# Kernel tuning notes

Measured on AMD Instinct MI355X. Metric: run time of the kernel, lower is better.

The kernel has to match this reference:

```python
import jax, jax.numpy as jnp
import numpy as np

INPUT_DIM = 64
INNER_DIM = 64
BATCH = 32768


def setup_inputs() -> dict:
    key = jax.random.key(0)
    ks = jax.random.split(key, 9)
    D, I = INPUT_DIM, INNER_DIM
    s1 = 1.0  # Linear(1, inner): fan_in=1
    s2 = 1.0 / np.sqrt(I)
    sg1 = 1.0 / np.sqrt(D * I)
    sg2 = 1.0 / np.sqrt(I)
    return {
        "x": jax.random.normal(ks[0], (BATCH, D), dtype=jnp.float32),
        # per-feature psi params, stacked over feature dim D
        "W1": jax.random.uniform(ks[1], (D, I), jnp.float32, -s1, s1),   # Linear(1, inner) weight
        "b1": jax.random.uniform(ks[2], (D, I), jnp.float32, -s1, s1),
        "W2": jax.random.uniform(ks[3], (D, I, I), jnp.float32, -s2, s2),  # Linear(inner, inner)
        "b2": jax.random.uniform(ks[4], (D, I), jnp.float32, -s2, s2),
        # g params
        "Wg1": jax.random.uniform(ks[5], (D * I, I), jnp.float32, -sg1, sg1),
        "bg1": jax.random.uniform(ks[6], (I,), jnp.float32, -sg1, sg1),
        "Wg2": jax.random.uniform(ks[7], (I, 1), jnp.float32, -sg2, sg2),
        "bg2": jax.random.uniform(ks[8], (1,), jnp.float32, -sg2, sg2),
    }


def reference(x, W1, b1, W2, b2, Wg1, bg1, Wg2, bg2):
    B = x.shape[0]
    # all psi_i first layers as one broadcasted outer product: [B, D, I]
    h = jnp.tanh(x[:, :, None] * W1[None, :, :] + b1[None, :, :])
    # per-feature second Linear(inner, inner): batched matmul over D
    psi = jnp.einsum("bdi,dio->bdo", h, W2) + b2[None, :, :]
    psi_concat = psi.reshape(B, -1)  # [B, D*I] == torch.cat over features
    hg = jnp.tanh(psi_concat @ Wg1 + bg1)
    out = hg @ Wg2 + bg2  # [B, 1]
    return out
```

## Files before the change

kernel.cpp:

```cpp
#include <hip/hip_runtime.h>
#include <stdint.h>

#define BATCH 32768
#define TANH_C 2.8853900817779268f

typedef __attribute__((ext_vector_type(8))) short short8;
typedef __attribute__((ext_vector_type(4))) float f32x4;
typedef __attribute__((ext_vector_type(4))) unsigned int u32x4;

__device__ __forceinline__ uint16_t bf16_rtne(float f) {
    union { float f; uint32_t u; } v; v.f = f;
    uint32_t u = v.u;
    u += 0x7fffu + ((u >> 16) & 1u);
    return (uint16_t)(u >> 16);
}

#if defined(__has_builtin)
#if __has_builtin(__builtin_amdgcn_cvt_pk_bf16_f32)
#define HAVE_CVT_PK_BF16 1
#endif
#endif

__device__ __forceinline__ uint32_t pack2_bf16(float a, float b) {
#ifdef HAVE_CVT_PK_BF16
    auto v = __builtin_amdgcn_cvt_pk_bf16_f32(a, b);
    uint32_t r; __builtin_memcpy(&r, &v, 4); return r;
#else
    return (uint32_t)bf16_rtne(a) | ((uint32_t)bf16_rtne(b) << 16);
#endif
}

__device__ __forceinline__ uint32_t tanh2_pack(float a, float b) {
    float ea = __builtin_amdgcn_exp2f(a);
    float eb = __builtin_amdgcn_exp2f(b);
    float da = 1.0f + ea, db = 1.0f + eb;
    float ir = __builtin_amdgcn_rcpf(da * db);
    float ha = fmaf(-2.0f * db, ir, 1.0f);
    float hb = fmaf(-2.0f * da, ir, 1.0f);
    return pack2_bf16(ha, hb);
}

__device__ __forceinline__ float fast_tanh(float x) {
    float e = __builtin_amdgcn_exp2f(x * TANH_C);
    return 1.0f - 2.0f * __builtin_amdgcn_rcpf(1.0f + e);
}

__global__ __launch_bounds__(512) void kol_pack(const float* __restrict__ W2,
                                                const float* __restrict__ Wg1,
                                                const float* __restrict__ b2,
                                                uint16_t* __restrict__ Bp,
                                                float* __restrict__ cgpart) {
    __shared__ __align__(16) float w2t[64 * 65];
    __shared__ __align__(16) float g1s[64 * 64];

    const int t = threadIdx.x;
    const int d = blockIdx.x;

    for (int f = t * 4; f < 4096; f += 2048) {
        float4 v = *(const float4*)&W2[(size_t)d * 4096 + f];
        int j = f >> 6, o = f & 63;
        w2t[(o + 0) * 65 + j] = v.x;
        w2t[(o + 1) * 65 + j] = v.y;
        w2t[(o + 2) * 65 + j] = v.z;
        w2t[(o + 3) * 65 + j] = v.w;
        *(float4*)&g1s[f] = *(const float4*)&Wg1[(size_t)d * 4096 + f];
    }
    __syncthreads();

    const int jg = t >> 6;
    const int n  = t & 63;
    float acc[8];
#pragma unroll
    for (int i = 0; i < 8; ++i) acc[i] = 0.f;

#pragma unroll 4
    for (int o = 0; o < 64; ++o) {
        float g = g1s[o * 64 + n];
        const float* w = &w2t[o * 65 + jg * 8];
#pragma unroll
        for (int jj = 0; jj < 8; ++jj) acc[jj] = fmaf(w[jj], g, acc[jj]);
    }

    u32x4 pk;
    pk.x = pack2_bf16(acc[0], acc[1]);
    pk.y = pack2_bf16(acc[2], acc[3]);
    pk.z = pack2_bf16(acc[4], acc[5]);
    pk.w = pack2_bf16(acc[6], acc[7]);
    int off = ((d * 2 + (jg >> 2)) * 4 + (n >> 4)) * 64 + (jg & 3) * 16 + (n & 15);
    ((u32x4*)Bp)[off] = pk;

    if (t < 64) {
        float a = 0.f;
        const float* b2d = &b2[(size_t)d * 64];
#pragma unroll 4
        for (int o = 0; o < 64; ++o)
            a = fmaf(b2d[o], g1s[o * 64 + t], a);
        cgpart[d * 64 + t] = a;
    }
}

__global__ __launch_bounds__(256) void kol_reduce_cg(const float* __restrict__ cgpart,
                                                     const float* __restrict__ bg1,
                                                     float* __restrict__ cg) {
    __shared__ float red[4][64];
    const int t = threadIdx.x;
    const int n = t & 63, seg = t >> 6;
    float a = 0.f;
#pragma unroll 4
    for (int d = seg * 16; d < seg * 16 + 16; ++d)
        a += cgpart[d * 64 + n];
    red[seg][n] = a;
    __syncthreads();
    if (t < 64)
        cg[n] = bg1[n] + red[0][n] + red[1][n] + red[2][n] + red[3][n];
}

__global__ __launch_bounds__(512, 4) void kol_main(
    const float* __restrict__ x, const float* __restrict__ W1, const float* __restrict__ b1,
    const uint16_t* __restrict__ Bp, const float* __restrict__ cg,
    const float* __restrict__ Wg2, const float* __restrict__ bg2f,
    float* __restrict__ out) {
    __shared__ __align__(16) float xs[64 * 68];
    __shared__ __align__(16) float w1s[4096];
    __shared__ __align__(16) float b1s[4096];

    const int tid = threadIdx.x;
    const int wave = tid >> 6, lane = tid & 63;
    const int quad = lane >> 4, lm = lane & 15;
    const int w4 = wave & 3, kh = wave >> 2;
    const int rowbase = blockIdx.x * 64;

#pragma unroll
    for (int ff = 0; ff < 2; ++ff) {
        int f = tid * 4 + ff * 2048;
        int r = f >> 6, c = f & 63;
        float4 v = *(const float4*)&x[(size_t)(rowbase + r) * 64 + c];
        v.x *= TANH_C; v.y *= TANH_C; v.z *= TANH_C; v.w *= TANH_C;
        *(float4*)&xs[r * 68 + c] = v;
        *(float4*)&w1s[f] = *(const float4*)&W1[f];
        float4 b = *(const float4*)&b1[f];
        b.x *= TANH_C; b.y *= TANH_C; b.z *= TANH_C; b.w *= TANH_C;
        *(float4*)&b1s[f] = b;
    }
    __syncthreads();

    f32x4 acc[4];
#pragma unroll
    for (int nt = 0; nt < 4; ++nt) acc[nt] = (f32x4){0.f, 0.f, 0.f, 0.f};

    const int dlo = kh * 32;
    const int myrow = w4 * 16 + lm;
    const float* xrow = &xs[myrow * 68];
    const short8* bbase = (const short8*)Bp + lane;

    short8 bf[8];
    {
        const short8* bp0 = bbase + (size_t)dlo * 512;
#pragma unroll
        for (int i = 0; i < 8; ++i) bf[i] = bp0[i * 64];
    }

#pragma unroll 2
    for (int dd = 0; dd < 32; ++dd) {
        const int d = dlo + dd;
        short8 bn[8];
        const short8* bpn = bbase + (size_t)(dlo + ((dd + 1) & 31)) * 512;
#pragma unroll
        for (int i = 0; i < 8; ++i) bn[i] = bpn[i * 64];

        const float xv = xrow[d];
        const float* wq = &w1s[d * 64 + quad * 8];
        const float* bq = &b1s[d * 64 + quad * 8];
        float4 wA = *(const float4*)&wq[0];
        float4 wB = *(const float4*)&wq[4];
        float4 wC = *(const float4*)&wq[32];
        float4 wD = *(const float4*)&wq[36];
        float4 bA = *(const float4*)&bq[0];
        float4 bB = *(const float4*)&bq[4];
        float4 bC = *(const float4*)&bq[32];
        float4 bD = *(const float4*)&bq[36];

        union { short8 s; uint32_t u[4]; } a0, a1;
        a0.u[0] = tanh2_pack(fmaf(xv, wA.x, bA.x), fmaf(xv, wA.y, bA.y));
        a0.u[1] = tanh2_pack(fmaf(xv, wA.z, bA.z), fmaf(xv, wA.w, bA.w));
        a0.u[2] = tanh2_pack(fmaf(xv, wB.x, bB.x), fmaf(xv, wB.y, bB.y));
        a0.u[3] = tanh2_pack(fmaf(xv, wB.z, bB.z), fmaf(xv, wB.w, bB.w));
        a1.u[0] = tanh2_pack(fmaf(xv, wC.x, bC.x), fmaf(xv, wC.y, bC.y));
        a1.u[1] = tanh2_pack(fmaf(xv, wC.z, bC.z), fmaf(xv, wC.w, bC.w));
        a1.u[2] = tanh2_pack(fmaf(xv, wD.x, bD.x), fmaf(xv, wD.y, bD.y));
        a1.u[3] = tanh2_pack(fmaf(xv, wD.z, bD.z), fmaf(xv, wD.w, bD.w));

#pragma unroll
        for (int nt = 0; nt < 4; ++nt)
            acc[nt] = __builtin_amdgcn_mfma_f32_16x16x32_bf16(a0.s, bf[nt], acc[nt], 0, 0, 0);
#pragma unroll
        for (int nt = 0; nt < 4; ++nt)
            acc[nt] = __builtin_amdgcn_mfma_f32_16x16x32_bf16(a1.s, bf[4 + nt], acc[nt], 0, 0, 0);

#pragma unroll
        for (int i = 0; i < 8; ++i) bf[i] = bn[i];
    }

    __syncthreads();
    float* cmb = xs;
    if (kh == 1) {
        int cb = (w4 * 64 + lane) * 17;
#pragma unroll
        for (int nt = 0; nt < 4; ++nt) *(f32x4*)&cmb[cb + nt * 4] = acc[nt];
    }
    __syncthreads();

    if (kh == 0) {
        int cb = (w4 * 64 + lane) * 17;
#pragma unroll
        for (int nt = 0; nt < 4; ++nt) {
            f32x4 o = *(const f32x4*)&cmb[cb + nt * 4];
            acc[nt] = acc[nt] + o;
        }
        float wg2v[4], cgv[4];
#pragma unroll
        for (int nt = 0; nt < 4; ++nt) {
            wg2v[nt] = Wg2[nt * 16 + lm];
            cgv[nt]  = cg[nt * 16 + lm];
        }
        const float bg2 = bg2f[0];
#pragma unroll
        for (int r = 0; r < 4; ++r) {
            float s = 0.f;
#pragma unroll
            for (int nt = 0; nt < 4; ++nt)
                s += wg2v[nt] * fast_tanh(acc[nt][r] + cgv[nt]);
            s += __shfl_xor(s, 1, 64);
            s += __shfl_xor(s, 2, 64);
            s += __shfl_xor(s, 4, 64);
            s += __shfl_xor(s, 8, 64);
            if (lm == 0) {
                int row = rowbase + w4 * 16 + quad * 4 + r;
                out[row] = s + bg2;
            }
        }
    }
}

extern "C" void kernel_launch(void* const* d_in, const int* in_sizes, int n_in,
                              void* d_out, int out_size, void* d_ws, size_t ws_size,
                              hipStream_t stream) {
    const float* x   = (const float*)d_in[0];
    const float* W1  = (const float*)d_in[1];
    const float* b1  = (const float*)d_in[2];
    const float* W2  = (const float*)d_in[3];
    const float* b2  = (const float*)d_in[4];
    const float* Wg1 = (const float*)d_in[5];
    const float* bg1 = (const float*)d_in[6];
    const float* Wg2 = (const float*)d_in[7];
    const float* bg2 = (const float*)d_in[8];
    float* out = (float*)d_out;

    uint16_t* Bp  = (uint16_t*)d_ws;
    float* cg     = (float*)((char*)d_ws + 4096 * 64 * 2);
    float* cgpart = out;

    kol_pack<<<64, 512, 0, stream>>>(W2, Wg1, b2, Bp, cgpart);
    kol_reduce_cg<<<1, 256, 0, stream>>>(cgpart, bg1, cg);
    kol_main<<<BATCH / 64, 512, 0, stream>>>(x, W1, b1, Bp, cg, Wg2, bg2, out);
}
```

Baseline: 126.9 us.

## Switch main kernel to 32x32x16 MFMA with 4-way K split across waves

```diff
diff --git a/kernel.cpp b/kernel.cpp
--- a/kernel.cpp
+++ b/kernel.cpp
@@ -6,6 +6,7 @@
 
 typedef __attribute__((ext_vector_type(8))) short short8;
 typedef __attribute__((ext_vector_type(4))) float f32x4;
+typedef __attribute__((ext_vector_type(16))) float f32x16;
 typedef __attribute__((ext_vector_type(4))) unsigned int u32x4;
 
 __device__ __forceinline__ uint16_t bf16_rtne(float f) {
@@ -86,7 +87,7 @@
     pk.y = pack2_bf16(acc[2], acc[3]);
     pk.z = pack2_bf16(acc[4], acc[5]);
     pk.w = pack2_bf16(acc[6], acc[7]);
-    int off = ((d * 2 + (jg >> 2)) * 4 + (n >> 4)) * 64 + (jg & 3) * 16 + (n & 15);
+    int off = ((d * 4 + (jg >> 1)) * 2 + (n >> 5)) * 64 + ((jg & 1) << 5) + (n & 31);
     ((u32x4*)Bp)[off] = pk;
 
     if (t < 64) {
@@ -120,14 +121,15 @@
     const uint16_t* __restrict__ Bp, const float* __restrict__ cg,
     const float* __restrict__ Wg2, const float* __restrict__ bg2f,
     float* __restrict__ out) {
-    __shared__ __align__(16) float xs[64 * 68];
-    __shared__ __align__(16) float w1s[4096];
-    __shared__ __align__(16) float b1s[4096];
+    __shared__ __align__(16) float smem[12544];
+    float* xs  = smem;
+    float* w1s = smem + 4352;
+    float* b1s = smem + 8448;
 
     const int tid = threadIdx.x;
     const int wave = tid >> 6, lane = tid & 63;
-    const int quad = lane >> 4, lm = lane & 15;
-    const int w4 = wave & 3, kh = wave >> 2;
+    const int nn = lane & 31, hi = lane >> 5;
+    const int rg = wave & 1, kq = wave >> 1;
     const int rowbase = blockIdx.x * 64;
 
 #pragma unroll
@@ -144,100 +146,98 @@
     }
     __syncthreads();
 
-    f32x4 acc[4];
-#pragma unroll
-    for (int nt = 0; nt < 4; ++nt) acc[nt] = (f32x4){0.f, 0.f, 0.f, 0.f};
-
-    const int dlo = kh * 32;
-    const int myrow = w4 * 16 + lm;
-    const float* xrow = &xs[myrow * 68];
-    const short8* bbase = (const short8*)Bp + lane;
-
-    short8 bf[8];
-    {
-        const short8* bp0 = bbase + (size_t)dlo * 512;
-#pragma unroll
-        for (int i = 0; i < 8; ++i) bf[i] = bp0[i * 64];
-    }
+    f32x16 acc0 = {0.f}, acc1 = {0.f};
+#pragma unroll
+    for (int i = 0; i < 16; ++i) { acc0[i] = 0.f; acc1[i] = 0.f; }
+
+    const u32x4* bp = (const u32x4*)Bp + lane;
+    const float* xcol = &xs[(rg * 32 + nn) * 68];
 
 #pragma unroll 2
-    for (int dd = 0; dd < 32; ++dd) {
-        const int d = dlo + dd;
-        short8 bn[8];
-        const short8* bpn = bbase + (size_t)(dlo + ((dd + 1) & 31)) * 512;
-#pragma unroll
-        for (int i = 0; i < 8; ++i) bn[i] = bpn[i * 64];
-
-        const float xv = xrow[d];
-        const float* wq = &w1s[d * 64 + quad * 8];
-        const float* bq = &b1s[d * 64 + quad * 8];
-        float4 wA = *(const float4*)&wq[0];
-        float4 wB = *(const float4*)&wq[4];
-        float4 wC = *(const float4*)&wq[32];
-        float4 wD = *(const float4*)&wq[36];
-        float4 bA = *(const float4*)&bq[0];
-        float4 bB = *(const float4*)&bq[4];
-        float4 bC = *(const float4*)&bq[32];
-        float4 bD = *(const float4*)&bq[36];
-
-        union { short8 s; uint32_t u[4]; } a0, a1;
-        a0.u[0] = tanh2_pack(fmaf(xv, wA.x, bA.x), fmaf(xv, wA.y, bA.y));
-        a0.u[1] = tanh2_pack(fmaf(xv, wA.z, bA.z), fmaf(xv, wA.w, bA.w));
-        a0.u[2] = tanh2_pack(fmaf(xv, wB.x, bB.x), fmaf(xv, wB.y, bB.y));
-        a0.u[3] = tanh2_pack(fmaf(xv, wB.z, bB.z), fmaf(xv, wB.w, bB.w));
-        a1.u[0] = tanh2_pack(fmaf(xv, wC.x, bC.x), fmaf(xv, wC.y, bC.y));
-        a1.u[1] = tanh2_pack(fmaf(xv, wC.z, bC.z), fmaf(xv, wC.w, bC.w));
-        a1.u[2] = tanh2_pack(fmaf(xv, wD.x, bD.x), fmaf(xv, wD.y, bD.y));
-        a1.u[3] = tanh2_pack(fmaf(xv, wD.z, bD.z), fmaf(xv, wD.w, bD.w));
-
-#pragma unroll
-        for (int nt = 0; nt < 4; ++nt)
-            acc[nt] = __builtin_amdgcn_mfma_f32_16x16x32_bf16(a0.s, bf[nt], acc[nt], 0, 0, 0);
-#pragma unroll
-        for (int nt = 0; nt < 4; ++nt)
-            acc[nt] = __builtin_amdgcn_mfma_f32_16x16x32_bf16(a1.s, bf[4 + nt], acc[nt], 0, 0, 0);
-
-#pragma unroll
-        for (int i = 0; i < 8; ++i) bf[i] = bn[i];
-    }
-
-    __syncthreads();
-    float* cmb = xs;
-    if (kh == 1) {
-        int cb = (w4 * 64 + lane) * 17;
-#pragma unroll
-        for (int nt = 0; nt < 4; ++nt) *(f32x4*)&cmb[cb + nt * 4] = acc[nt];
-    }
-    __syncthreads();
-
-    if (kh == 0) {
-        int cb = (w4 * 64 + lane) * 17;
-#pragma unroll
-        for (int nt = 0; nt < 4; ++nt) {
-            f32x4 o = *(const f32x4*)&cmb[cb + nt * 4];
-            acc[nt] = acc[nt] + o;
-        }
-        float wg2v[4], cgv[4];
-#pragma unroll
-        for (int nt = 0; nt < 4; ++nt) {
-            wg2v[nt] = Wg2[nt * 16 + lm];
-            cgv[nt]  = cg[nt * 16 + lm];
-        }
+    for (int dd = 0; dd < 16; ++dd) {
+        const int d = kq * 16 + dd;
+        const u32x4* bfp = bp + (size_t)d * 512;
+        u32x4 bfr[8];
+#pragma unroll
+        for (int i = 0; i < 8; ++i) bfr[i] = bfp[i * 64];
+
+        const float xv = xcol[d];
+        short8 afr[4];
+#pragma unroll
+        for (int c = 0; c < 4; ++c) {
+            const float* wq = &w1s[d * 64 + c * 16 + hi * 8];
+            const float* bq = &b1s[d * 64 + c * 16 + hi * 8];
+            float4 w0 = *(const float4*)&wq[0];
+            float4 w1v = *(const float4*)&wq[4];
+            float4 b0 = *(const float4*)&bq[0];
+            float4 b1v = *(const float4*)&bq[4];
+            union { short8 s; uint32_t u[4]; } a;
+            a.u[0] = tanh2_pack(fmaf(xv, w0.x, b0.x), fmaf(xv, w0.y, b0.y));
+            a.u[1] = tanh2_pack(fmaf(xv, w0.z, b0.z), fmaf(xv, w0.w, b0.w));
+            a.u[2] = tanh2_pack(fmaf(xv, w1v.x, b1v.x), fmaf(xv, w1v.y, b1v.y));
+            a.u[3] = tanh2_pack(fmaf(xv, w1v.z, b1v.z), fmaf(xv, w1v.w, b1v.w));
+            afr[c] = a.s;
+        }
+#pragma unroll
+        for (int c = 0; c < 4; ++c) {
+            union { u32x4 u; short8 s; } b0c, b1c;
+            b0c.u = bfr[c * 2 + 0];
+            b1c.u = bfr[c * 2 + 1];
+            acc0 = __builtin_amdgcn_mfma_f32_32x32x16_bf16(afr[c], b0c.s, acc0, 0, 0, 0);
+            acc1 = __builtin_amdgcn_mfma_f32_32x32x16_bf16(afr[c], b1c.s, acc1, 0, 0, 0);
+        }
+    }
+
+    __syncthreads();
+    f32x4* cmb = (f32x4*)smem;
+    if (kq != 0) {
+        const int widx = (kq - 1) * 2 + rg;
+#pragma unroll
+        for (int s = 0; s < 8; ++s) {
+            const int base = (s & 3) * 4;
+            f32x4 v;
+            if (s < 4) v = (f32x4){acc0[base], acc0[base + 1], acc0[base + 2], acc0[base + 3]};
+            else       v = (f32x4){acc1[base], acc1[base + 1], acc1[base + 2], acc1[base + 3]};
+            cmb[(s * 6 + widx) * 64 + lane] = v;
+        }
+    }
+    __syncthreads();
+
+    if (kq == 0) {
+#pragma unroll
+        for (int s = 0; s < 8; ++s) {
+            const int base = (s & 3) * 4;
+            f32x4 v0 = cmb[(s * 6 + 0 + rg) * 64 + lane];
+            f32x4 v1 = cmb[(s * 6 + 2 + rg) * 64 + lane];
+            f32x4 v2 = cmb[(s * 6 + 4 + rg) * 64 + lane];
+            f32x4 v = v0 + v1 + v2;
+            if (s < 4) {
+#pragma unroll
+                for (int i = 0; i < 4; ++i) acc0[base + i] += v[i];
+            } else {
+#pragma unroll
+                for (int i = 0; i < 4; ++i) acc1[base + i] += v[i];
+            }
+        }
+        const float cg0 = cg[nn],      cg1 = cg[32 + nn];
+        const float wg0 = Wg2[nn],     wg1 = Wg2[32 + nn];
         const float bg2 = bg2f[0];
 #pragma unroll
-        for (int r = 0; r < 4; ++r) {
-            float s = 0.f;
-#pragma unroll
-            for (int nt = 0; nt < 4; ++nt)
-                s += wg2v[nt] * fast_tanh(acc[nt][r] + cgv[nt]);
-            s += __shfl_xor(s, 1, 64);
-            s += __shfl_xor(s, 2, 64);
-            s += __shfl_xor(s, 4, 64);
-            s += __shfl_xor(s, 8, 64);
-            if (lm == 0) {
-                int row = rowbase + w4 * 16 + quad * 4 + r;
-                out[row] = s + bg2;
+        for (int g = 0; g < 4; ++g) {
+            float4 res;
+#pragma unroll
+            for (int rr = 0; rr < 4; ++rr) {
+                const int r = g * 4 + rr;
+                float s = wg0 * fast_tanh(acc0[r] + cg0) + wg1 * fast_tanh(acc1[r] + cg1);
+                s += __shfl_xor(s, 1, 64);
+                s += __shfl_xor(s, 2, 64);
+                s += __shfl_xor(s, 4, 64);
+                s += __shfl_xor(s, 8, 64);
+                s += __shfl_xor(s, 16, 64);
+                ((float*)&res)[rr] = s + bg2;
             }
+            if (nn == 0)
+                *(float4*)&out[rowbase + rg * 32 + 8 * g + 4 * hi] = res;
         }
     }
 }
```

Result: faster. 124.3 us (-2.0%).
